# Performance work log

Measured on AMD Instinct MI355X. Metric: run time of the kernel, lower is better.

Reference implementation:

```python
import jax, jax.numpy as jnp
import numpy as np
from jax import lax

BS, H, W, NA = 128, 64, 64, 4
C1, C2, HID = 16, 32, 512

def setup_inputs() -> dict:
    key = jax.random.key(0)
    ks = jax.random.split(key, 12)
    s = 0.05
    return {
        "diffs": jax.random.uniform(ks[0], (BS, NA, 2), jnp.float32) * 4.0,  # agent locations
        "states": jax.random.normal(ks[1], (BS, NA * 3, H, W), jnp.float32),
        "conv1_w": jax.random.normal(ks[2], (C1, 3, 8, 8), jnp.float32) * s,
        "conv1_b": jnp.zeros((C1,), jnp.float32),
        "conv2_w": jax.random.normal(ks[3], (C2, C1, 5, 5), jnp.float32) * s,
        "conv2_b": jnp.zeros((C2,), jnp.float32),
        "g_w": jax.random.normal(ks[4], (HID, 2 * C2 + 2), jnp.float32) * s,
        "g_b": jnp.zeros((HID,), jnp.float32),
        "fc4_w": jax.random.normal(ks[5], (2, HID), jnp.float32) * s,
        "fc4_b": jnp.zeros((2,), jnp.float32),
        "fc5_w": jax.random.normal(ks[6], (1, HID), jnp.float32) * s,
        "fc5_b": jnp.zeros((1,), jnp.float32),
    }

def _conv(x, w, b):
    y = lax.conv_general_dilated(x, w, (1, 1), 'VALID',
                                 dimension_numbers=('NCHW', 'OIHW', 'NCHW'))
    return jax.nn.relu(y + b[None, :, None, None])

def reference(diffs, states, conv1_w, conv1_b, conv2_w, conv2_b,
              g_w, g_b, fc4_w, fc4_b, fc5_w, fc5_b):
    bs = states.shape[0]
    # ---- encoder: per-agent CNN + global max pool ----
    x = states.reshape(bs * NA, 3, H, W)
    x = _conv(x, conv1_w, conv1_b)
    x = _conv(x, conv2_w, conv2_b)
    feat = jnp.max(x, axis=(2, 3)).reshape(bs, NA, C2)  # (bs, 4, 32)
    # ---- coordinator: adjacency from pairwise location diffs ----
    locs = diffs
    pdiffs = locs[:, :, None, :] - locs[:, None, :, :]  # (bs, 4, 4, 2)
    norms = jnp.linalg.norm(pdiffs, axis=-1)
    thresh = jnp.linalg.norm(jnp.array([1.0, 1.0], jnp.float32))
    A = (norms < thresh).astype(jnp.float32)
    A = A / jnp.clip(jnp.sum(A, axis=-1, keepdims=True), 1e-6)  # row-normalized adjacency
    mask = 1.0 - jnp.eye(NA, dtype=jnp.float32)  # messages skip j == i
    Am = A * mask  # (bs, 4, 4)
    # ---- CatEdgeGraphLayer: h_i = relu(W [f_i ; sum_j A_ij [f_j ; d_ij]] + b) ----
    feat_agg = jnp.einsum('bij,bjc->bic', Am, feat)          # (bs, 4, 32)
    diff_agg = jnp.einsum('bij,bijd->bid', Am, pdiffs)       # (bs, 4, 2)
    h = jnp.concatenate([feat, feat_agg, diff_agg], axis=-1)  # (bs, 4, 66)
    h = jax.nn.relu(jnp.einsum('bic,oc->bio', h, g_w) + g_b)  # (bs, 4, 512)
    policies = jnp.einsum('bic,oc->bio', h, fc4_w) + fc4_b    # (bs, 4, 2)
    values = jnp.einsum('bic,oc->bio', h, fc5_w) + fc5_b      # (bs, 4, 1)
    return (policies, values)
```

## Files before the change

### kernel.cpp

```cpp
#include <hip/hip_runtime.h>
#include <hip/hip_bf16.h>

#define H1 57
#define H2 53
#define XP 60
#define SIP 968

typedef _Float16 f16;
typedef _Float16 f16x4 __attribute__((ext_vector_type(4)));
typedef _Float16 f16x8 __attribute__((ext_vector_type(8)));
typedef float f32x4 __attribute__((ext_vector_type(4)));
typedef float f32x16 __attribute__((ext_vector_type(16)));

__global__ __launch_bounds__(256) void k_repack(const float* __restrict__ w1,
    const float* __restrict__ w2, const float* __restrict__ gw,
    f16* __restrict__ w1f, f16* __restrict__ w2f,
    float2* __restrict__ gwT2, float* __restrict__ feat)
{
  const int tid = blockIdx.x * 256 + threadIdx.x;
  const int stride = 32 * 256;
  for (int i = tid; i < 8 * 64 * 8; i += stride) {
    int j = i & 7;
    int l = (i >> 3) & 63;
    int tp = i >> 9;
    int c = j & 3;
    int kw = 2 * (l >> 4) + (j >> 2);
    int oc = l & 15;
    float v = (c < 3) ? w1[((oc * 3 + c) * 8 + tp) * 8 + kw] : 0.f;
    w1f[i] = (f16)v;
  }
  for (int i = tid; i < 25 * 64 * 8; i += stride) {
    int j = i & 7;
    int l = (i >> 3) & 63;
    int tap = i >> 9;
    int oc = l & 31;
    int ch = ((l >> 5) << 3) + j;
    w2f[i] = (f16)w2[((oc * 16 + ch) * 5 + tap / 5) * 5 + tap % 5];
  }
  for (int i = tid; i < 66 * 256; i += stride) {
    int t = i & 255;
    int c = i >> 8;
    float2 v;
    v.x = gw[(2 * t) * 66 + c];
    v.y = gw[(2 * t + 1) * 66 + c];
    gwT2[i] = v;
  }
  for (int i = tid; i < 512 * 32; i += stride) feat[i] = 0.f;
}

__global__ __launch_bounds__(256) void k_conv1(const float* __restrict__ in,
    const f16* __restrict__ w1f, const float* __restrict__ b1,
    f16* __restrict__ O1)
{
  __shared__ __align__(16) f16 sIn[23][72][4];
  const int img = blockIdx.x;
  const int y0 = min((int)blockIdx.y * 16, 41);
  const int lane = threadIdx.x & 63;
  const int wv = threadIdx.x >> 6;

  f16x8 Bf[8];
  #pragma unroll
  for (int tp = 0; tp < 8; ++tp)
    Bf[tp] = *(const f16x8*)&w1f[(tp * 64 + lane) * 8];

  for (int i = threadIdx.x; i < 23 * 16; i += 256) {
    int y = i >> 4, xq = i & 15;
    int yy = min(y0 + y, 63);
    const float* p0 = &in[(((size_t)img * 3 + 0) * 64 + yy) * 64 + xq * 4];
    float4 v0 = *(const float4*)p0;
    float4 v1 = *(const float4*)(p0 + 4096);
    float4 v2 = *(const float4*)(p0 + 8192);
    float c0[4] = {v0.x, v0.y, v0.z, v0.w};
    float c1[4] = {v1.x, v1.y, v1.z, v1.w};
    float c2[4] = {v2.x, v2.y, v2.z, v2.w};
    #pragma unroll
    for (int q = 0; q < 4; ++q) {
      f16x4 tt = {(f16)c0[q], (f16)c1[q], (f16)c2[q], (f16)0.f};
      *(f16x4*)&sIn[y][xq * 4 + q][0] = tt;
    }
  }
  for (int i = threadIdx.x; i < 23 * 8; i += 256) {
    int y = i >> 3, xi = i & 7;
    *(f16x4*)&sIn[y][64 + xi][0] = (f16x4){(f16)0.f, (f16)0.f, (f16)0.f, (f16)0.f};
  }
  __syncthreads();

  const int g = lane >> 4;
  const int n16 = lane & 15;

  const f32x4 biasv = {b1[g * 4 + 0], b1[g * 4 + 1], b1[g * 4 + 2], b1[g * 4 + 3]};
  f32x4 acc[4][4];
  #pragma unroll
  for (int r = 0; r < 4; ++r)
    #pragma unroll
    for (int xt = 0; xt < 4; ++xt)
      acc[r][xt] = biasv;

  #pragma unroll
  for (int row = 0; row <= 10; ++row) {
    const int prow = 4 * wv + row;
    f16x8 a[4];
    #pragma unroll
    for (int xt = 0; xt < 4; ++xt)
      a[xt] = *(const f16x8*)&sIn[prow][xt * 16 + n16 + 2 * g][0];
    #pragma unroll
    for (int r = 0; r < 4; ++r) {
      const int tp = row - r;
      if (tp >= 0 && tp < 8) {
        #pragma unroll
        for (int xt = 0; xt < 4; ++xt)
          acc[r][xt] = __builtin_amdgcn_mfma_f32_16x16x32_f16(Bf[tp], a[xt], acc[r][xt], 0, 0, 0);
      }
    }
  }

  #pragma unroll
  for (int r = 0; r < 4; ++r) {
    const int yy = y0 + 4 * wv + r;
    f16* rowp = &O1[(((size_t)img * H1 + yy) * 2 + (g >> 1)) * XP * 8 + (g & 1) * 4];
    #pragma unroll
    for (int xt = 0; xt < 4; ++xt) {
      const int px = xt * 16 + n16;
      if (px < H1) {
        f16x4 v;
        #pragma unroll
        for (int q = 0; q < 4; ++q) v[q] = (f16)fmaxf(acc[r][xt][q], 0.f);
        *(f16x4*)&rowp[px * 8] = v;
      }
    }
  }
}

__global__ __launch_bounds__(256, 4) void k_conv2(const f16* __restrict__ O1,
    const f16* __restrict__ w2f, const float* __restrict__ b2,
    float* __restrict__ feat)
{
  __shared__ __align__(16) f16 sW[16 * 64 * 8];
  __shared__ __align__(16) f16 sI[12 * SIP + 16];
  __shared__ unsigned smax[32];
  const int img = blockIdx.x;
  const int y0 = min((int)blockIdx.y * 8, 45);
  const int lane = threadIdx.x & 63;
  const int wv = threadIdx.x >> 6;
  if (threadIdx.x < 32) smax[threadIdx.x] = 0u;

  f16x8 Br[9];
  const f16* pBg = &w2f[lane * 8];
  #pragma unroll
  for (int t = 0; t < 9; ++t)
    Br[t] = *(const f16x8*)(pBg + t * 512);

  for (int i = threadIdx.x; i < 16 * 64; i += 256)
    ((float4*)sW)[i] = ((const float4*)w2f)[9 * 64 + i];
  {
    const float4* src = (const float4*)(O1 + (size_t)(img * H1 + y0) * (2 * XP * 8));
    for (int i = threadIdx.x; i < 1440; i += 256) {
      int y = i / 120;
      int rem = i - y * 120;
      ((float4*)&sI[y * SIP])[rem] = src[i];
    }
  }
  __syncthreads();

  const int m32 = lane & 31;
  const int G = lane >> 5;

  const int start = (wv < 2) ? wv * 4 : 8 + (wv - 2) * 3;
  const int cnt = (wv < 2) ? 4 : 3;

  const float bias = b2[m32];
  f32x16 acc[4];
  #pragma unroll
  for (int ti = 0; ti < 4; ++ti)
    #pragma unroll
    for (int q = 0; q < 16; ++q)
      acc[ti][q] = bias;

  const f16* pA[4];
  #pragma unroll
  for (int ti = 0; ti < 4; ++ti) {
    int t = start + ti;
    int p = t * 32 + m32;
    p = min(p, 423);
    int y = (p * 1237) >> 16;
    int x = p - 53 * y;
    pA[ti] = &sI[y * SIP + G * 480 + x * 8];
  }

  #pragma unroll
  for (int tap = 0; tap < 25; ++tap) {
    const int kh = tap / 5, kw = tap % 5;
    const int off = kh * SIP + kw * 8;
    f16x8 Bv = (tap < 9) ? Br[tap] : *(const f16x8*)(&sW[lane * 8] + (tap - 9) * 512);
    #pragma unroll
    for (int ti = 0; ti < 4; ++ti) {
      if (ti < cnt) {
        f16x8 Av = *(const f16x8*)(pA[ti] + off);
        acc[ti] = __builtin_amdgcn_mfma_f32_32x32x16_f16(Av, Bv, acc[ti], 0, 0, 0);
      }
    }
  }

  float m = 0.f;
  #pragma unroll
  for (int ti = 0; ti < 4; ++ti) {
    if (ti < cnt) {
      const int t = start + ti;
      #pragma unroll
      for (int q = 0; q < 16; ++q) {
        if (t == 13 && q >= 4) continue;
        m = fmaxf(m, acc[ti][q]);
      }
    }
  }
  m = fmaxf(m, 0.f);
  m = fmaxf(m, __shfl_xor(m, 32, 64));
  if (lane < 32) atomicMax(&smax[m32], __float_as_uint(m));
  __syncthreads();
  if (threadIdx.x < 32)
    atomicMax((unsigned*)&feat[img * 32 + threadIdx.x], smax[threadIdx.x]);
}

__global__ __launch_bounds__(256) void k_head(const float* __restrict__ diffs,
    const float* __restrict__ feat, const float2* __restrict__ gwT2,
    const float* __restrict__ gb, const float* __restrict__ w4,
    const float* __restrict__ b4, const float* __restrict__ w5,
    const float* __restrict__ b5, float* __restrict__ out)
{
  __shared__ float h66[4][66];
  __shared__ float hout[4][512];
  __shared__ float Am[4][4];
  __shared__ float pd[4][4][2];
  __shared__ float fs[4][32];
  const int b = blockIdx.x;
  const int tid = threadIdx.x;
  if (tid < 128) {
    int i = tid >> 5, c = tid & 31;
    fs[i][c] = feat[(b * 4 + i) * 32 + c];
  }
  if (tid == 0) {
    float lx[4], ly[4];
    #pragma unroll
    for (int a = 0; a < 4; ++a) {
      lx[a] = diffs[(b * 4 + a) * 2];
      ly[a] = diffs[(b * 4 + a) * 2 + 1];
    }
    #pragma unroll
    for (int i = 0; i < 4; ++i) {
      float A[4];
      float rs = 0.f;
      #pragma unroll
      for (int j = 0; j < 4; ++j) {
        float dx = lx[i] - lx[j], dy = ly[i] - ly[j];
        pd[i][j][0] = dx;
        pd[i][j][1] = dy;
        float n = sqrtf(dx * dx + dy * dy);
        A[j] = (n < 1.41421356237309504880f) ? 1.f : 0.f;
        rs += A[j];
      }
      float inv = 1.f / fmaxf(rs, 1e-6f);
      #pragma unroll
      for (int j = 0; j < 4; ++j)
        Am[i][j] = (i == j) ? 0.f : A[j] * inv;
    }
  }
  __syncthreads();
  if (tid < 128) {
    int i = tid >> 5, c = tid & 31;
    h66[i][c] = fs[i][c];
    float s = 0.f;
    #pragma unroll
    for (int j = 0; j < 4; ++j) s += Am[i][j] * fs[j][c];
    h66[i][32 + c] = s;
  } else if (tid < 136) {
    int q = tid - 128;
    int i = q >> 1, d = q & 1;
    float s = 0.f;
    #pragma unroll
    for (int j = 0; j < 4; ++j) s += Am[i][j] * pd[i][j][d];
    h66[i][64 + d] = s;
  }
  __syncthreads();
  {
    const float b0 = gb[2 * tid], b1g = gb[2 * tid + 1];
    float a[4][2];
    #pragma unroll
    for (int i = 0; i < 4; ++i) { a[i][0] = b0; a[i][1] = b1g; }
    #pragma unroll 6
    for (int c = 0; c < 66; ++c) {
      float2 w = gwT2[c * 256 + tid];
      #pragma unroll
      for (int i = 0; i < 4; ++i) {
        float h = h66[i][c];
        a[i][0] = fmaf(h, w.x, a[i][0]);
        a[i][1] = fmaf(h, w.y, a[i][1]);
      }
    }
    #pragma unroll
    for (int i = 0; i < 4; ++i) {
      float2 v;
      v.x = fmaxf(a[i][0], 0.f);
      v.y = fmaxf(a[i][1], 0.f);
      *(float2*)&hout[i][2 * tid] = v;
    }
  }
  __syncthreads();
  if (tid < 192) {
    int gq = tid >> 4, l = tid & 15;
    int i = gq / 3, k = gq % 3;
    const float* wrow = (k < 2) ? &w4[k * 512] : w5;
    float s = 0.f;
    for (int o = l; o < 512; o += 16) s = fmaf(hout[i][o], wrow[o], s);
    #pragma unroll
    for (int d = 8; d >= 1; d >>= 1) s += __shfl_xor(s, d, 16);
    if (l == 0) {
      if (k < 2) out[(b * 4 + i) * 2 + k] = s + b4[k];
      else       out[1024 + b * 4 + i] = s + b5[0];
    }
  }
}

extern "C" void kernel_launch(void* const* d_in, const int* in_sizes, int n_in,
                              void* d_out, int out_size, void* d_ws, size_t ws_size,
                              hipStream_t stream) {
  const float* diffs  = (const float*)d_in[0];
  const float* states = (const float*)d_in[1];
  const float* w1 = (const float*)d_in[2];
  const float* b1 = (const float*)d_in[3];
  const float* w2 = (const float*)d_in[4];
  const float* b2 = (const float*)d_in[5];
  const float* gw = (const float*)d_in[6];
  const float* gb = (const float*)d_in[7];
  const float* w4 = (const float*)d_in[8];
  const float* b4 = (const float*)d_in[9];
  const float* w5 = (const float*)d_in[10];
  const float* b5 = (const float*)d_in[11];
  float* out = (float*)d_out;

  char* base = (char*)d_ws;
  f16*    w1f  = (f16*)base;
  f16*    w2f  = (f16*)(base + 8192);
  float2* gwT2 = (float2*)(base + 34816);
  float*  feat = (float*)(base + 169984);
  f16*    O1   = (f16*)(base + 235520);

  k_repack<<<32, 256, 0, stream>>>(w1, w2, gw, w1f, w2f, gwT2, feat);
  k_conv1<<<dim3(512, 4), 256, 0, stream>>>(states, w1f, b1, O1);
  k_conv2<<<dim3(512, 7), 256, 0, stream>>>(O1, w2f, b2, feat);
  k_head<<<128, 256, 0, stream>>>(diffs, feat, gwT2, gb, w4, b4, w5, b5, out);
}
```

Measured before the change: 86.92 us.

## Fold weight repack into conv1, tighten O1 row padding, batch conv2 A loads

Removes the separate repack kernel launch. Each conv1 block now builds its own f16 conv1 weight fragments in shared memory, and the row-0 blocks handle the conv2 weight, gw transpose and feat zeroing in a grid-stride loop. The O1 intermediate row padding shrinks from 60 to 57 pixels, which reduces global traffic and conv2 shared-memory staging. The conv2 inner loop now issues all A loads before the MFMAs and raises wave priority around the MFMA burst. In exchange, conv1 blocks do redundant weight conversion work, and the tighter LDS stride may change bank-conflict behavior.

New measurement: 88.87 us. 2.2% more time.

```diff
diff --git a/kernel.cpp b/kernel.cpp
--- a/kernel.cpp
+++ b/kernel.cpp
@@ -3,8 +3,9 @@
 
 #define H1 57
 #define H2 53
-#define XP 60
-#define SIP 968
+#define XP 57
+#define OROW 912
+#define SIP 920
 
 typedef _Float16 f16;
 typedef _Float16 f16x4 __attribute__((ext_vector_type(4)));
@@ -12,56 +13,49 @@
 typedef float f32x4 __attribute__((ext_vector_type(4)));
 typedef float f32x16 __attribute__((ext_vector_type(16)));
 
-__global__ __launch_bounds__(256) void k_repack(const float* __restrict__ w1,
-    const float* __restrict__ w2, const float* __restrict__ gw,
-    f16* __restrict__ w1f, f16* __restrict__ w2f,
+__global__ __launch_bounds__(256) void k_conv1(const float* __restrict__ in,
+    const float* __restrict__ w1, const float* __restrict__ b1,
+    f16* __restrict__ O1, const float* __restrict__ w2,
+    const float* __restrict__ gw, f16* __restrict__ w2f,
     float2* __restrict__ gwT2, float* __restrict__ feat)
 {
-  const int tid = blockIdx.x * 256 + threadIdx.x;
-  const int stride = 32 * 256;
-  for (int i = tid; i < 8 * 64 * 8; i += stride) {
-    int j = i & 7;
-    int l = (i >> 3) & 63;
-    int tp = i >> 9;
-    int c = j & 3;
-    int kw = 2 * (l >> 4) + (j >> 2);
-    int oc = l & 15;
-    float v = (c < 3) ? w1[((oc * 3 + c) * 8 + tp) * 8 + kw] : 0.f;
-    w1f[i] = (f16)v;
-  }
-  for (int i = tid; i < 25 * 64 * 8; i += stride) {
-    int j = i & 7;
-    int l = (i >> 3) & 63;
-    int tap = i >> 9;
-    int oc = l & 31;
-    int ch = ((l >> 5) << 3) + j;
-    w2f[i] = (f16)w2[((oc * 16 + ch) * 5 + tap / 5) * 5 + tap % 5];
-  }
-  for (int i = tid; i < 66 * 256; i += stride) {
-    int t = i & 255;
-    int c = i >> 8;
-    float2 v;
-    v.x = gw[(2 * t) * 66 + c];
-    v.y = gw[(2 * t + 1) * 66 + c];
-    gwT2[i] = v;
-  }
-  for (int i = tid; i < 512 * 32; i += stride) feat[i] = 0.f;
-}
-
-__global__ __launch_bounds__(256) void k_conv1(const float* __restrict__ in,
-    const f16* __restrict__ w1f, const float* __restrict__ b1,
-    f16* __restrict__ O1)
-{
   __shared__ __align__(16) f16 sIn[23][72][4];
+  __shared__ __align__(16) f16 sWf[8 * 64 * 8];
   const int img = blockIdx.x;
-  const int y0 = min((int)blockIdx.y * 16, 41);
+  const int by = blockIdx.y;
+  const int y0 = min(by * 16, 41);
   const int lane = threadIdx.x & 63;
   const int wv = threadIdx.x >> 6;
 
-  f16x8 Bf[8];
-  #pragma unroll
-  for (int tp = 0; tp < 8; ++tp)
-    Bf[tp] = *(const f16x8*)&w1f[(tp * 64 + lane) * 8];
+  if (by == 0) {
+    const int t0 = img * 256 + threadIdx.x;
+    const int stride = 512 * 256;
+    for (int i = t0; i < 25 * 64 * 8; i += stride) {
+      int j = i & 7, l = (i >> 3) & 63, tap = i >> 9;
+      int oc = l & 31, ch = ((l >> 5) << 3) + j;
+      w2f[i] = (f16)w2[((oc * 16 + ch) * 5 + tap / 5) * 5 + tap % 5];
+    }
+    for (int i = t0; i < 66 * 256; i += stride) {
+      int t = i & 255, c = i >> 8;
+      float2 v;
+      v.x = gw[(2 * t) * 66 + c];
+      v.y = gw[(2 * t + 1) * 66 + c];
+      gwT2[i] = v;
+    }
+    for (int i = t0; i < 512 * 32; i += stride) feat[i] = 0.f;
+  }
+
+  for (int pr = threadIdx.x; pr < 512; pr += 256) {
+    int l = pr & 63, tp = pr >> 6;
+    int kwb = 2 * (l >> 4), oc = l & 15;
+    f16x8 v;
+    #pragma unroll
+    for (int j = 0; j < 8; ++j) {
+      int c = j & 3, kw = kwb + (j >> 2);
+      v[j] = (f16)((c < 3) ? w1[((oc * 3 + c) * 8 + tp) * 8 + kw] : 0.f);
+    }
+    *(f16x8*)&sWf[pr * 8] = v;
+  }
 
   for (int i = threadIdx.x; i < 23 * 16; i += 256) {
     int y = i >> 4, xq = i & 15;
@@ -88,6 +82,11 @@
   const int g = lane >> 4;
   const int n16 = lane & 15;
 
+  f16x8 Bf[8];
+  #pragma unroll
+  for (int tp = 0; tp < 8; ++tp)
+    Bf[tp] = *(const f16x8*)&sWf[(tp * 64 + lane) * 8];
+
   const f32x4 biasv = {b1[g * 4 + 0], b1[g * 4 + 1], b1[g * 4 + 2], b1[g * 4 + 3]};
   f32x4 acc[4][4];
   #pragma unroll
@@ -117,7 +116,7 @@
   #pragma unroll
   for (int r = 0; r < 4; ++r) {
     const int yy = y0 + 4 * wv + r;
-    f16* rowp = &O1[(((size_t)img * H1 + yy) * 2 + (g >> 1)) * XP * 8 + (g & 1) * 4];
+    f16* rowp = &O1[(size_t)(img * H1 + yy) * OROW + (g >> 1) * (XP * 8) + (g & 1) * 4];
     #pragma unroll
     for (int xt = 0; xt < 4; ++xt) {
       const int px = xt * 16 + n16;
@@ -153,10 +152,10 @@
   for (int i = threadIdx.x; i < 16 * 64; i += 256)
     ((float4*)sW)[i] = ((const float4*)w2f)[9 * 64 + i];
   {
-    const float4* src = (const float4*)(O1 + (size_t)(img * H1 + y0) * (2 * XP * 8));
-    for (int i = threadIdx.x; i < 1440; i += 256) {
-      int y = i / 120;
-      int rem = i - y * 120;
+    const float4* src = (const float4*)(O1 + (size_t)(img * H1 + y0) * OROW);
+    for (int i = threadIdx.x; i < 12 * 114; i += 256) {
+      int y = i / 114;
+      int rem = i - y * 114;
       ((float4*)&sI[y * SIP])[rem] = src[i];
     }
   }
@@ -184,7 +183,7 @@
     p = min(p, 423);
     int y = (p * 1237) >> 16;
     int x = p - 53 * y;
-    pA[ti] = &sI[y * SIP + G * 480 + x * 8];
+    pA[ti] = &sI[y * SIP + G * (XP * 8) + x * 8];
   }
 
   #pragma unroll
@@ -192,13 +191,16 @@
     const int kh = tap / 5, kw = tap % 5;
     const int off = kh * SIP + kw * 8;
     f16x8 Bv = (tap < 9) ? Br[tap] : *(const f16x8*)(&sW[lane * 8] + (tap - 9) * 512);
-    #pragma unroll
-    for (int ti = 0; ti < 4; ++ti) {
-      if (ti < cnt) {
-        f16x8 Av = *(const f16x8*)(pA[ti] + off);
-        acc[ti] = __builtin_amdgcn_mfma_f32_32x32x16_f16(Av, Bv, acc[ti], 0, 0, 0);
-      }
-    }
+    f16x8 Av[4];
+    #pragma unroll
+    for (int ti = 0; ti < 4; ++ti)
+      if (ti < cnt) Av[ti] = *(const f16x8*)(pA[ti] + off);
+    __builtin_amdgcn_s_setprio(1);
+    #pragma unroll
+    for (int ti = 0; ti < 4; ++ti)
+      if (ti < cnt)
+        acc[ti] = __builtin_amdgcn_mfma_f32_32x32x16_f16(Av[ti], Bv, acc[ti], 0, 0, 0);
+    __builtin_amdgcn_s_setprio(0);
   }
 
   float m = 0.f;
@@ -338,14 +340,12 @@
   float* out = (float*)d_out;
 
   char* base = (char*)d_ws;
-  f16*    w1f  = (f16*)base;
-  f16*    w2f  = (f16*)(base + 8192);
-  float2* gwT2 = (float2*)(base + 34816);
-  float*  feat = (float*)(base + 169984);
-  f16*    O1   = (f16*)(base + 235520);
-
-  k_repack<<<32, 256, 0, stream>>>(w1, w2, gw, w1f, w2f, gwT2, feat);
-  k_conv1<<<dim3(512, 4), 256, 0, stream>>>(states, w1f, b1, O1);
+  f16*    w2f  = (f16*)base;
+  float2* gwT2 = (float2*)(base + 32768);
+  float*  feat = (float*)(base + 167936);
+  f16*    O1   = (f16*)(base + 233472);
+
+  k_conv1<<<dim3(512, 4), 256, 0, stream>>>(states, w1, b1, O1, w2, gw, w2f, gwT2, feat);
   k_conv2<<<dim3(512, 7), 256, 0, stream>>>(O1, w2f, b2, feat);
   k_head<<<128, 256, 0, stream>>>(diffs, feat, gwT2, gb, w4, b4, w5, b5, out);
 }
```
